# Optimization experiments

Measured on AMD Instinct MI355X. Metric: run time of the kernel, lower is better.

Reference implementation:

```python
import jax, jax.numpy as jnp
import numpy as np

B = 256        # batch of LLR frames
N = 576        # code length (from wman_N0576_R34_z24)
MR = 144       # check rows = N * (1 - 3/4)
Z = 24         # lifting factor
IT = 3         # decoding iterations
ROW_DEG = 15   # check-node degree (WiMAX rate-3/4)


def setup_inputs() -> dict:
    key = jax.random.key(0)
    r = jax.random.normal(key, (B, N), dtype=jnp.float32)
    # Deterministic sparse Tanner graph: 15 ones per check row (>=2 required for top-2)
    rng = np.random.RandomState(0)
    Hnp = np.zeros((MR, N), dtype=np.int32)
    cols = np.argsort(rng.rand(MR, N), axis=1)[:, :ROW_DEG]
    Hnp[np.arange(MR)[:, None], cols] = 1
    H = jnp.asarray(Hnp)
    alpha = jnp.ones((MR // Z, N // Z, IT), dtype=jnp.float32) * 0.7
    beta = jnp.ones((MR // Z, N // Z, IT), dtype=jnp.float32) * 0.05
    return {"r": r, "alpha": alpha, "beta": beta, "H": H}


def _decode(r, alpha, beta, Hf):
    # r: (B, N) channel LLRs; Hf: (MR, N) float 0/1 parity-check mask
    mask = Hf == 1.0
    node = jnp.arange(N)[None, None, :]           # (1, 1, N)
    M = Hf[None, :, :] * r[:, None, :]            # initial v->c messages (B, MR, N)
    E = jnp.zeros_like(M)
    n_it = alpha.shape[-1]
    for it in range(n_it):
        a = jnp.repeat(jnp.repeat(alpha[:, :, it], Z, axis=0), Z, axis=1)  # (MR, N)
        bt = jnp.repeat(jnp.repeat(beta[:, :, it], Z, axis=0), Z, axis=1)  # (MR, N)
        # check -> variable: masked min-2 magnitude + extrinsic sign product
        abs_M = jnp.abs(M)
        masked = jnp.where(mask, abs_M, jnp.inf)
        neg_vals, idx = jax.lax.top_k(-masked, 2)  # two smallest per check row
        min_vals = -neg_vals                        # (B, MR, 2)
        # exclude self: use 2nd min at the argmin position, 1st min elsewhere
        E_abs = jnp.where(node == idx[..., 0:1], min_vals[..., 1:2], min_vals[..., 0:1])
        signs = jnp.where(mask, jnp.sign(M), 1.0)
        row_sign_prod = jnp.prod(signs, axis=2, keepdims=True)
        E_sign = row_sign_prod * signs              # extrinsic sign
        E = a * E_sign * jax.nn.relu(E_abs - bt) * Hf
        # variable -> check: sum-minus-self
        sum_E = jnp.sum(E, axis=1, keepdims=True)   # (B, 1, N)
        M = (r[:, None, :] + sum_E - E) * Hf
    return r + jnp.sum(E, axis=1)                   # posterior LLRs (B, N)


def reference(r, alpha, beta, H):
    return _decode(r, alpha, beta, H.astype(jnp.float32))
```

## Files before the change

kernel.cpp:

```cpp
#include <hip/hip_runtime.h>

#define BATCH   256
#define NCOL    576
#define MROW    144
#define ZLIFT   24
#define NIT     3
#define ROW_DEG 15
#define PKSTR   16
#define NSCIT   ((MROW/ZLIFT) * (NCOL/ZLIFT) * NIT)
#define TPB     576
#define CCAP    17
#define CSTR    20

__global__ __launch_bounds__(256) void build_cols_kernel(
    const int* __restrict__ H, int* __restrict__ pk)
{
    const int wave = (blockIdx.x * blockDim.x + threadIdx.x) >> 6;
    const int lane = threadIdx.x & 63;
    if (wave >= MROW) return;
    const int4* row4 = (const int4*)(H + (size_t)wave * NCOL);
    const int srow = (wave / ZLIFT) * (NCOL / ZLIFT);
    const unsigned long long below = (1ull << lane) - 1ull;
    if (lane == 0) pk[wave * PKSTR + 15] = 0;

    int4 h[3];
    #pragma unroll
    for (int r0 = 0; r0 < 3; ++r0) {
        const int vidx = r0 * 64 + lane;
        h[r0] = make_int4(0, 0, 0, 0);
        if (vidx < NCOL / 4) h[r0] = row4[vidx];
    }

    int base = 0;
    #pragma unroll
    for (int r0 = 0; r0 < 3; ++r0) {
        const int b0 = h[r0].x != 0, b1 = h[r0].y != 0;
        const int b2 = h[r0].z != 0, b3 = h[r0].w != 0;
        const unsigned long long m0 = __ballot(b0);
        const unsigned long long m1 = __ballot(b1);
        const unsigned long long m2 = __ballot(b2);
        const unsigned long long m3 = __ballot(b3);
        const int cnt_below = __popcll(m0 & below) + __popcll(m1 & below)
                            + __popcll(m2 & below) + __popcll(m3 & below);
        const int bits[4] = {b0, b1, b2, b3};
        const int n0 = (r0 * 64 + lane) * 4;
        int pref = 0;
        #pragma unroll
        for (int c = 0; c < 4; ++c) {
            if (bits[c]) {
                const int idx = base + cnt_below + pref;
                const int n = n0 + c;
                if (idx < ROW_DEG)
                    pk[wave * PKSTR + idx] = n | (((srow + n / ZLIFT) * NIT) << 16);
                ++pref;
            }
        }
        base += __popcll(m0) + __popcll(m1) + __popcll(m2) + __popcll(m3);
    }
}

__global__ __launch_bounds__(TPB) void ldpc_decode_kernel(
    const float* __restrict__ r,
    const float* __restrict__ alpha,
    const float* __restrict__ beta,
    const int*   __restrict__ pk,
    float*       __restrict__ out)
{
    __shared__ float  r_s[NCOL];
    __shared__ float  colsum[NCOL];
    __shared__ __align__(16) float E_s[NCOL * CSTR];
    __shared__ float2 ab_s[NSCIT];
    __shared__ int    cdeg[NCOL];

    const int b   = blockIdx.x;
    const int tid = threadIdx.x;
    const int row = tid >> 2;
    const int sub = tid & 3;

    const int4  q  = *(const int4*)(pk + row * PKSTR + sub * 4);
    const float rv = r[(size_t)b * NCOL + tid];
    float2 abv;
    if (tid < NSCIT) abv = make_float2(alpha[tid], beta[tid]);

    r_s[tid]  = rv;
    cdeg[tid] = 0;
    {
        float4* E4 = (float4*)E_s;
        const float4 z4 = make_float4(0.f, 0.f, 0.f, 0.f);
        #pragma unroll
        for (int j = 0; j < CSTR / 4; ++j) E4[j * NCOL + tid] = z4;
    }
    if (tid < NSCIT) ab_s[tid] = abv;
    __syncthreads();

    int pk_r[4] = {q.x, q.y, q.z, q.w};
    float r_r[4], E_r[4];
    int   slot_r[4];
    #pragma unroll
    for (int j = 0; j < 4; ++j) {
        const int kglob = sub * 4 + j;
        const int n = pk_r[j] & 0xFFFF;
        r_r[j] = r_s[n];
        E_r[j] = 0.0f;
        if (kglob < ROW_DEG)
            slot_r[j] = n * CSTR + atomicAdd(&cdeg[n], 1);
    }

    for (int it = 0; it < NIT; ++it) {
        float vals[4];
        float min1 = INFINITY, min2 = INFINITY;
        int   kmin = 1 << 30;
        float sprod = 1.0f;
        #pragma unroll
        for (int j = 0; j < 4; ++j) {
            const int kglob = sub * 4 + j;
            const bool val = (kglob < ROW_DEG);
            float v;
            if (it == 0) {
                v = r_r[j];
            } else {
                const int n = pk_r[j] & 0xFFFF;
                v = r_r[j] + colsum[n] - E_r[j];
            }
            vals[j] = v;
            const float av = val ? fabsf(v) : INFINITY;
            const float s = val ? ((v > 0.0f) ? 1.0f : ((v < 0.0f) ? -1.0f : 0.0f))
                                : 1.0f;
            sprod *= s;
            if (av < min1)      { min2 = min1; min1 = av; kmin = kglob; }
            else if (av < min2) { min2 = av; }
        }
        float2 ab_e[4];
        #pragma unroll
        for (int j = 0; j < 4; ++j) {
            const int kglob = sub * 4 + j;
            if (kglob < ROW_DEG) ab_e[j] = ab_s[(pk_r[j] >> 16) + it];
        }
        #pragma unroll
        for (int m = 1; m <= 2; m <<= 1) {
            const float o1 = __shfl_xor(min1, m);
            const float o2 = __shfl_xor(min2, m);
            const int   ok = __shfl_xor(kmin, m);
            const float os = __shfl_xor(sprod, m);
            const bool self_lo = ((sub & m) == 0);
            const float lo1 = self_lo ? min1 : o1;
            const float lo2 = self_lo ? min2 : o2;
            const int   lok = self_lo ? kmin : ok;
            const float hi1 = self_lo ? o1 : min1;
            const float hi2 = self_lo ? o2 : min2;
            const int   hik = self_lo ? ok : kmin;
            if (hi1 < lo1) { min1 = hi1; kmin = hik; min2 = fminf(hi2, lo1); }
            else           { min1 = lo1; kmin = lok; min2 = fminf(lo2, hi1); }
            sprod *= os;
        }
        #pragma unroll
        for (int j = 0; j < 4; ++j) {
            const int kglob = sub * 4 + j;
            if (kglob < ROW_DEG) {
                const float v = vals[j];
                const float s = (v > 0.0f) ? 1.0f : ((v < 0.0f) ? -1.0f : 0.0f);
                const float eabs = (kglob == kmin) ? min2 : min1;
                float mag = eabs - ab_e[j].y;
                if (mag < 0.0f) mag = 0.0f;
                const float E = ab_e[j].x * (sprod * s) * mag;
                E_r[j] = E;
                E_s[slot_r[j]] = E;
            }
        }
        __syncthreads();

        const float4* b4 = (const float4*)(&E_s[tid * CSTR]);
        const float4 x0 = b4[0];
        const float4 x1 = b4[1];
        const float4 x2 = b4[2];
        const float4 x3 = b4[3];
        const float  x4 = E_s[tid * CSTR + 16];
        const float4 t01 = make_float4(x0.x + x1.x, x0.y + x1.y,
                                       x0.z + x1.z, x0.w + x1.w);
        const float4 t23 = make_float4(x2.x + x3.x, x2.y + x3.y,
                                       x2.z + x3.z, x2.w + x3.w);
        const float4 t = make_float4(t01.x + t23.x, t01.y + t23.y,
                                     t01.z + t23.z, t01.w + t23.w);
        const float sum = ((t.x + t.y) + (t.z + t.w)) + x4;
        if (it < NIT - 1) {
            colsum[tid] = sum;
            __syncthreads();
        } else {
            out[(size_t)b * NCOL + tid] = r_s[tid] + sum;
        }
    }
}

extern "C" void kernel_launch(void* const* d_in, const int* in_sizes, int n_in,
                              void* d_out, int out_size, void* d_ws, size_t ws_size,
                              hipStream_t stream) {
    const float* r     = (const float*)d_in[0];
    const float* alpha = (const float*)d_in[1];
    const float* beta  = (const float*)d_in[2];
    const int*   H     = (const int*)d_in[3];
    float* out = (float*)d_out;
    int*   pk  = (int*)d_ws;

    build_cols_kernel<<<(MROW * 64 + 255) / 256, 256, 0, stream>>>(H, pk);
    ldpc_decode_kernel<<<BATCH, TPB, 0, stream>>>(r, alpha, beta, pk, out);
}
```

Baseline: 65.47 us.

## Fuse H column-index build into the decode kernel via shared memory

```diff
diff --git a/kernel.cpp b/kernel.cpp
--- a/kernel.cpp
+++ b/kernel.cpp
@@ -12,58 +12,11 @@
 #define CCAP    17
 #define CSTR    20
 
-__global__ __launch_bounds__(256) void build_cols_kernel(
-    const int* __restrict__ H, int* __restrict__ pk)
-{
-    const int wave = (blockIdx.x * blockDim.x + threadIdx.x) >> 6;
-    const int lane = threadIdx.x & 63;
-    if (wave >= MROW) return;
-    const int4* row4 = (const int4*)(H + (size_t)wave * NCOL);
-    const int srow = (wave / ZLIFT) * (NCOL / ZLIFT);
-    const unsigned long long below = (1ull << lane) - 1ull;
-    if (lane == 0) pk[wave * PKSTR + 15] = 0;
-
-    int4 h[3];
-    #pragma unroll
-    for (int r0 = 0; r0 < 3; ++r0) {
-        const int vidx = r0 * 64 + lane;
-        h[r0] = make_int4(0, 0, 0, 0);
-        if (vidx < NCOL / 4) h[r0] = row4[vidx];
-    }
-
-    int base = 0;
-    #pragma unroll
-    for (int r0 = 0; r0 < 3; ++r0) {
-        const int b0 = h[r0].x != 0, b1 = h[r0].y != 0;
-        const int b2 = h[r0].z != 0, b3 = h[r0].w != 0;
-        const unsigned long long m0 = __ballot(b0);
-        const unsigned long long m1 = __ballot(b1);
-        const unsigned long long m2 = __ballot(b2);
-        const unsigned long long m3 = __ballot(b3);
-        const int cnt_below = __popcll(m0 & below) + __popcll(m1 & below)
-                            + __popcll(m2 & below) + __popcll(m3 & below);
-        const int bits[4] = {b0, b1, b2, b3};
-        const int n0 = (r0 * 64 + lane) * 4;
-        int pref = 0;
-        #pragma unroll
-        for (int c = 0; c < 4; ++c) {
-            if (bits[c]) {
-                const int idx = base + cnt_below + pref;
-                const int n = n0 + c;
-                if (idx < ROW_DEG)
-                    pk[wave * PKSTR + idx] = n | (((srow + n / ZLIFT) * NIT) << 16);
-                ++pref;
-            }
-        }
-        base += __popcll(m0) + __popcll(m1) + __popcll(m2) + __popcll(m3);
-    }
-}
-
-__global__ __launch_bounds__(TPB) void ldpc_decode_kernel(
+__global__ __launch_bounds__(TPB) void ldpc_fused_kernel(
     const float* __restrict__ r,
     const float* __restrict__ alpha,
     const float* __restrict__ beta,
-    const int*   __restrict__ pk,
+    const int*   __restrict__ H,
     float*       __restrict__ out)
 {
     __shared__ float  r_s[NCOL];
@@ -71,16 +24,69 @@
     __shared__ __align__(16) float E_s[NCOL * CSTR];
     __shared__ float2 ab_s[NSCIT];
     __shared__ int    cdeg[NCOL];
-
-    const int b   = blockIdx.x;
-    const int tid = threadIdx.x;
-    const int row = tid >> 2;
-    const int sub = tid & 3;
-
-    const int4  q  = *(const int4*)(pk + row * PKSTR + sub * 4);
+    __shared__ int    pk_s[MROW * PKSTR];
+
+    const int b    = blockIdx.x;
+    const int tid  = threadIdx.x;
+    const int row  = tid >> 2;
+    const int sub  = tid & 3;
+    const int wid  = tid >> 6;
+    const int lane = tid & 63;
+
     const float rv = r[(size_t)b * NCOL + tid];
     float2 abv;
     if (tid < NSCIT) abv = make_float2(alpha[tid], beta[tid]);
+
+    const unsigned long long below = (1ull << lane) - 1ull;
+    #pragma unroll
+    for (int chunk = 0; chunk < 4; ++chunk) {
+        int4 h[4][3];
+        #pragma unroll
+        for (int rr = 0; rr < 4; ++rr) {
+            const int m = wid * 16 + chunk * 4 + rr;
+            const int4* row4 = (const int4*)(H + (size_t)m * NCOL);
+            #pragma unroll
+            for (int r0 = 0; r0 < 3; ++r0) {
+                const int vidx = r0 * 64 + lane;
+                h[rr][r0] = make_int4(0, 0, 0, 0);
+                if (vidx < NCOL / 4) h[rr][r0] = row4[vidx];
+            }
+        }
+        #pragma unroll
+        for (int rr = 0; rr < 4; ++rr) {
+            const int m = wid * 16 + chunk * 4 + rr;
+            if (lane == 0) pk_s[m * PKSTR + 15] = 0;
+            const int srow = (m / ZLIFT) * (NCOL / ZLIFT);
+            int base = 0;
+            #pragma unroll
+            for (int r0 = 0; r0 < 3; ++r0) {
+                const int b0 = h[rr][r0].x != 0, b1 = h[rr][r0].y != 0;
+                const int b2 = h[rr][r0].z != 0, b3 = h[rr][r0].w != 0;
+                const unsigned long long m0 = __ballot(b0);
+                const unsigned long long m1 = __ballot(b1);
+                const unsigned long long m2 = __ballot(b2);
+                const unsigned long long m3 = __ballot(b3);
+                const int cnt_below = __popcll(m0 & below) + __popcll(m1 & below)
+                                    + __popcll(m2 & below) + __popcll(m3 & below);
+                const int bits[4] = {b0, b1, b2, b3};
+                const int n0 = (r0 * 64 + lane) * 4;
+                int pref = 0;
+                #pragma unroll
+                for (int c = 0; c < 4; ++c) {
+                    if (bits[c]) {
+                        const int idx = base + cnt_below + pref;
+                        const int n = n0 + c;
+                        if (idx < ROW_DEG)
+                            pk_s[m * PKSTR + idx] =
+                                n | (((srow + n / ZLIFT) * NIT) << 16);
+                        ++pref;
+                    }
+                }
+                base += __popcll(m0) + __popcll(m1)
+                      + __popcll(m2) + __popcll(m3);
+            }
+        }
+    }
 
     r_s[tid]  = rv;
     cdeg[tid] = 0;
@@ -93,6 +99,7 @@
     if (tid < NSCIT) ab_s[tid] = abv;
     __syncthreads();
 
+    const int4 q = *(const int4*)(&pk_s[row * PKSTR + sub * 4]);
     int pk_r[4] = {q.x, q.y, q.z, q.w};
     float r_r[4], E_r[4];
     int   slot_r[4];
@@ -199,8 +206,7 @@
     const float* beta  = (const float*)d_in[2];
     const int*   H     = (const int*)d_in[3];
     float* out = (float*)d_out;
-    int*   pk  = (int*)d_ws;
-
-    build_cols_kernel<<<(MROW * 64 + 255) / 256, 256, 0, stream>>>(H, pk);
-    ldpc_decode_kernel<<<BATCH, TPB, 0, stream>>>(r, alpha, beta, pk, out);
+    (void)d_ws; (void)ws_size;
+
+    ldpc_fused_kernel<<<BATCH, TPB, 0, stream>>>(r, alpha, beta, H, out);
 }
```

New measurement: 78.58 us. 20.0% more time.
